# Performance work log

Measured on AMD Instinct MI355X. Metric: run time of the kernel, lower is better.

The kernel has to match this reference:

```python
import jax, jax.numpy as jnp
import numpy as np

B, S, D = 2, 4096, 768
H, DH = 12, 64
W = 256          # one-sided window (attention_window=512 // 2)
G = 8            # number of global tokens (first G positions)
NEG = -1e9


def setup_inputs() -> dict:
    key = jax.random.key(0)
    ks = jax.random.split(key, 8)
    hidden_states = jax.random.normal(ks[0], (B, S, D), dtype=jnp.float32)
    attention_mask = jnp.ones((B, S), dtype=jnp.float32)
    sc = 0.02
    Wq = jax.random.normal(ks[1], (D, D), dtype=jnp.float32) * sc
    Wk = jax.random.normal(ks[2], (D, D), dtype=jnp.float32) * sc
    Wv = jax.random.normal(ks[3], (D, D), dtype=jnp.float32) * sc
    Wqg = jax.random.normal(ks[4], (D, D), dtype=jnp.float32) * sc
    Wkg = jax.random.normal(ks[5], (D, D), dtype=jnp.float32) * sc
    Wvg = jax.random.normal(ks[6], (D, D), dtype=jnp.float32) * sc
    return {"hidden_states": hidden_states, "attention_mask": attention_mask,
            "Wq": Wq, "Wk": Wk, "Wv": Wv, "Wqg": Wqg, "Wkg": Wkg, "Wvg": Wvg}


def _heads(x):  # [B,S,D] -> [B,H,S,DH]
    return x.reshape(B, S, H, DH).transpose(0, 2, 1, 3)


def longformer_attn(hidden_states, attention_mask, Wq, Wk, Wv, Wqg, Wkg, Wvg):
    scale = 1.0 / jnp.sqrt(jnp.float32(DH))
    q = _heads(hidden_states @ Wq) * scale   # [B,H,S,DH]
    k = _heads(hidden_states @ Wk)
    v = _heads(hidden_states @ Wv)

    n = S // W                                # number of query chunks
    kp = jnp.pad(k, ((0, 0), (0, 0), (W, W), (0, 0)))
    vp = jnp.pad(v, ((0, 0), (0, 0), (W, W), (0, 0)))
    # window indices into padded seq: chunk i covers keys [i*W - W, i*W + 2W)
    idx = jnp.arange(n)[:, None] * W + jnp.arange(3 * W)[None, :]   # [n,3W]
    k_win = kp[:, :, idx]                     # [B,H,n,3W,DH]
    v_win = vp[:, :, idx]
    qc = q.reshape(B, H, n, W, DH)

    scores = jnp.einsum('bhnqd,bhnkd->bhnqk', qc, k_win)  # [B,H,n,W,3W]

    # masks: band (|key-query|<=W), valid key position, not a global key,
    # and key attention_mask
    rel = jnp.arange(3 * W)[None, :] - jnp.arange(W)[:, None]   # [W,3W] = k - q
    band = (rel >= 0) & (rel <= 2 * W)
    key_pos = idx - W                                           # [n,3W] real positions
    valid = (key_pos >= 0) & (key_pos < S) & (key_pos >= G)
    struct_mask = band[None, :, :] & valid[:, None, :]          # [n,W,3W]
    amp = jnp.pad(attention_mask, ((0, 0), (W, W)))
    am_win = amp[:, idx] > 0.5                                  # [B,n,3W]
    full_mask = struct_mask[None] & am_win[:, :, None, :]       # [B,n,W,3W]
    scores = jnp.where(full_mask[:, None], scores, NEG)

    # every query also attends to the G global keys (regular key projection)
    gk = k[:, :, :G]                                            # [B,H,G,DH]
    gscore = jnp.einsum('bhsd,bhgd->bhsg', q, gk).reshape(B, H, n, W, G)
    all_scores = jnp.concatenate([gscore, scores], axis=-1)     # [B,H,n,W,G+3W]
    probs = jax.nn.softmax(all_scores, axis=-1)

    gv = v[:, :, :G]
    out = (jnp.einsum('bhnqk,bhnkd->bhnqd', probs[..., G:], v_win)
           + jnp.einsum('bhnqg,bhgd->bhnqd', probs[..., :G], gv))
    out = out.reshape(B, H, S, DH)

    # global queries attend to ALL tokens with the *_global projections
    qg = _heads(hidden_states @ Wqg)[:, :, :G] * scale          # [B,H,G,DH]
    kg = _heads(hidden_states @ Wkg)
    vg = _heads(hidden_states @ Wvg)
    gs = jnp.einsum('bhgd,bhsd->bhgs', qg, kg)                  # [B,H,G,S]
    gs = jnp.where(attention_mask[:, None, None, :] > 0.5, gs, NEG)
    gp = jax.nn.softmax(gs, axis=-1)
    gout = jnp.einsum('bhgs,bhsd->bhgd', gp, vg)
    out = out.at[:, :, :G].set(gout)

    return out.transpose(0, 2, 1, 3).reshape(B, S, D)


def reference(hidden_states, attention_mask, Wq, Wk, Wv, Wqg, Wkg, Wvg):
    return longformer_attn(hidden_states, attention_mask, Wq, Wk, Wv, Wqg, Wkg, Wvg)
```

## Files before the change

kernel.cpp:

```cpp
#include <hip/hip_runtime.h>

#define B_ 2
#define S_ 4096
#define D_ 768
#define H_ 12
#define DH_ 64
#define W_ 256
#define G_ 8
#define NEG_ (-1e9f)
#define NC_ 64
#define CK_ 64
#define WQB 128
#define NT_ 11

typedef __attribute__((ext_vector_type(4))) float f32x4;
typedef __attribute__((ext_vector_type(16))) float f32x16;
typedef __attribute__((ext_vector_type(8))) short s16x8;
typedef __attribute__((ext_vector_type(4))) short s16x4;
typedef unsigned short ushort_t;

__device__ __forceinline__ unsigned short f2bf(float f) {
    union { float f; unsigned u; } v; v.f = f;
    unsigned r = v.u + 0x7FFFu + ((v.u >> 16) & 1u);
    return (unsigned short)(r >> 16);
}
__device__ __forceinline__ float bf2f(unsigned short b) {
    union { unsigned u; float f; } v; v.u = ((unsigned)b) << 16;
    return v.f;
}
__device__ __forceinline__ unsigned cvtpk_bf16(float lo, float hi) {
    unsigned r;
    asm("v_cvt_pk_bf16_f32 %0, %1, %2" : "=v"(r) : "v"(lo), "v"(hi));
    return r;
}
__device__ __forceinline__ void gload16(const ushort_t* g, ushort_t* l) {
    __builtin_amdgcn_global_load_lds(
        (const __attribute__((address_space(1))) unsigned*)g,
        (__attribute__((address_space(3))) unsigned*)l, 16, 0, 0);
}

__global__ __launch_bounds__(256) void convert_hs(const float* __restrict__ x,
                                                  ushort_t* __restrict__ y, int n8) {
    int i = blockIdx.x * 256 + threadIdx.x;
    if (i >= n8) return;
    float4 a = *(const float4*)&x[(size_t)i * 8];
    float4 c = *(const float4*)&x[(size_t)i * 8 + 4];
    s16x8 o;
    o[0] = (short)f2bf(a.x); o[1] = (short)f2bf(a.y);
    o[2] = (short)f2bf(a.z); o[3] = (short)f2bf(a.w);
    o[4] = (short)f2bf(c.x); o[5] = (short)f2bf(c.y);
    o[6] = (short)f2bf(c.z); o[7] = (short)f2bf(c.w);
    *(s16x8*)&y[(size_t)i * 8] = o;
}

__global__ __launch_bounds__(256) void convert_wt(const float* __restrict__ W0,
                                                  const float* __restrict__ W1,
                                                  const float* __restrict__ W2,
                                                  const float* __restrict__ W3,
                                                  const float* __restrict__ W4,
                                                  ushort_t* __restrict__ wt) {
    __shared__ float tile[32][33];
    const int w = blockIdx.z;
    const float* Wsrc = (w == 0) ? W0 : (w == 1) ? W1 : (w == 2) ? W2 : (w == 3) ? W3 : W4;
    const float scl = (w == 0) ? 0.125f : 1.0f;
    const int k0 = blockIdx.x * 32;
    const int n0 = blockIdx.y * 32;
    const int t = threadIdx.x;
    const int r = t >> 3, c4 = (t & 7) * 4;
    float4 src = *(const float4*)&Wsrc[(size_t)(k0 + r) * D_ + n0 + c4];
    tile[r][c4 + 0] = src.x; tile[r][c4 + 1] = src.y;
    tile[r][c4 + 2] = src.z; tile[r][c4 + 3] = src.w;
    __syncthreads();
    s16x4 o;
    o[0] = (short)f2bf(tile[c4 + 0][r] * scl);
    o[1] = (short)f2bf(tile[c4 + 1][r] * scl);
    o[2] = (short)f2bf(tile[c4 + 2][r] * scl);
    o[3] = (short)f2bf(tile[c4 + 3][r] * scl);
    *(s16x4*)&wt[((size_t)(w * D_ + n0 + r)) * D_ + k0 + c4] = o;
}

__global__ __launch_bounds__(256, 2) void proj_mfma(const ushort_t* __restrict__ A,
                                                    const ushort_t* __restrict__ Bt,
                                                    ushort_t* __restrict__ oq,
                                                    ushort_t* __restrict__ ok,
                                                    ushort_t* __restrict__ ov,
                                                    ushort_t* __restrict__ okg,
                                                    ushort_t* __restrict__ ovg) {
    __shared__ char smem[34048];
    ushort_t* Al = (ushort_t*)smem;
    ushort_t* Bl = Al + 128 * 64;

    const int t = threadIdx.x;
    const int m0 = blockIdx.x * 128;
    const int n0 = blockIdx.y * 128;
    const int lane = t & 63;
    const int w = t >> 6;
    const int wm = (w >> 1) * 64, wn = (w & 1) * 64;
    const int ln = lane & 15, hi = lane >> 4;

    const int srow_in_call = lane >> 3;
    const int scol = ((lane & 7) ^ srow_in_call) * 8;

    f32x4 acc[4][4];
#pragma unroll
    for (int mi = 0; mi < 4; ++mi)
#pragma unroll
        for (int ni = 0; ni < 4; ++ni) acc[mi][ni] = (f32x4){0.f, 0.f, 0.f, 0.f};

    for (int k0 = 0; k0 < D_; k0 += 64) {
        __syncthreads();
#pragma unroll
        for (int j = 0; j < 4; ++j) {
            const int rbase = (w * 4 + j) * 8;
            const int row = rbase + srow_in_call;
            gload16(&A[(size_t)(m0 + row) * D_ + k0 + scol], &Al[rbase * 64]);
            gload16(&Bt[(size_t)(n0 + row) * D_ + k0 + scol], &Bl[rbase * 64]);
        }
        __syncthreads();

#pragma unroll
        for (int ks = 0; ks < 2; ++ks) {
            s16x8 af[4], bf[4];
#pragma unroll
            for (int i = 0; i < 4; ++i) {
                const int ar = wm + i * 16 + ln;
                const int br = wn + i * 16 + ln;
                const int slot = (4 * ks + hi) ^ (ln & 7);
                af[i] = *(const s16x8*)&Al[ar * 64 + slot * 8];
                bf[i] = *(const s16x8*)&Bl[br * 64 + slot * 8];
            }
#pragma unroll
            for (int mi = 0; mi < 4; ++mi)
#pragma unroll
                for (int ni = 0; ni < 4; ++ni)
                    acc[mi][ni] = __builtin_amdgcn_mfma_f32_16x16x32_bf16(af[mi], bf[ni], acc[mi][ni], 0, 0, 0);
        }
    }

    float* scr = (float*)smem;
    const int rl = t >> 2, cs = (t & 3) * 32;
    const int ng = n0 + cs;
    const int w_idx = ng / D_;
    const int cb = ng - w_idx * D_;
    const int hh = cb >> 6, dd = cb & 63;
    ushort_t* dst = (w_idx == 0) ? oq : (w_idx == 1) ? ok : (w_idx == 2) ? ov
                    : (w_idx == 3) ? okg : ovg;

#pragma unroll
    for (int r = 0; r < 2; ++r) {
        __syncthreads();
        if ((w >> 1) == r) {
#pragma unroll
            for (int mi = 0; mi < 4; ++mi)
#pragma unroll
                for (int ni = 0; ni < 4; ++ni)
#pragma unroll
                    for (int rr = 0; rr < 4; ++rr)
                        scr[(mi * 16 + hi * 4 + rr) * 132 + wn + ni * 16 + ln] = acc[mi][ni][rr];
        }
        __syncthreads();
        const int m = m0 + r * 64 + rl;
        const int bb = m >> 12, s = m & 4095;
        ushort_t* drow = dst + ((size_t)(bb * H_ + hh) * S_ + s) * DH_ + dd;
        const float* srcp = scr + rl * 132 + cs;
#pragma unroll
        for (int seg = 0; seg < 4; ++seg) {
            float4 lo = *(const float4*)&srcp[seg * 8];
            float4 hi4 = *(const float4*)&srcp[seg * 8 + 4];
            s16x8 o;
            o[0] = (short)f2bf(lo.x); o[1] = (short)f2bf(lo.y);
            o[2] = (short)f2bf(lo.z); o[3] = (short)f2bf(lo.w);
            o[4] = (short)f2bf(hi4.x); o[5] = (short)f2bf(hi4.y);
            o[6] = (short)f2bf(hi4.z); o[7] = (short)f2bf(hi4.w);
            *(s16x8*)&drow[seg * 8] = o;
        }
    }
}

__global__ __launch_bounds__(256) void qg_gemm(const float* __restrict__ X,
                                               const float* __restrict__ Wm,
                                               float* __restrict__ qg) {
    const int rp = blockIdx.x;
    const int c0 = blockIdx.y * 128;
    const int t = threadIdx.x;
    const int r = t >> 7, cl = t & 127;
    __shared__ float xr[2][D_];
    for (int i = t; i < 2 * D_; i += 256) {
        const int rr = i / D_, kk = i - rr * D_;
        const int row = rp * 2 + rr;
        const int b = row >> 3, g = row & 7;
        xr[rr][kk] = X[((size_t)b * S_ + g) * D_ + kk];
    }
    __syncthreads();
    float a0 = 0.f, a1 = 0.f, a2 = 0.f, a3 = 0.f;
    const float* wp = &Wm[c0 + cl];
    for (int kk = 0; kk < D_; kk += 4) {
        a0 += xr[r][kk + 0] * wp[(size_t)(kk + 0) * D_];
        a1 += xr[r][kk + 1] * wp[(size_t)(kk + 1) * D_];
        a2 += xr[r][kk + 2] * wp[(size_t)(kk + 2) * D_];
        a3 += xr[r][kk + 3] * wp[(size_t)(kk + 3) * D_];
    }
    const int row = rp * 2 + r;
    qg[(size_t)row * D_ + c0 + cl] = (a0 + a1 + a2 + a3) * 0.125f;
}

__global__ __launch_bounds__(256, 2) void win_mfma(const ushort_t* __restrict__ q,
                                                   const ushort_t* __restrict__ k,
                                                   const ushort_t* __restrict__ v,
                                                   const float* __restrict__ am,
                                                   float* __restrict__ out) {
    __shared__ char smem[34816];
    ushort_t* Kl = (ushort_t*)smem;
    ushort_t* Vt = Kl + 64 * 72;
    unsigned* Mv = (unsigned*)(Vt + 64 * 66);
    float* Ow = (float*)smem;

    const int n = blockIdx.x, h = blockIdx.y, b = blockIdx.z;
    const int t = threadIdx.x;
    const int lane = t & 63, w = t >> 6;
    const int l31 = lane & 31, h5 = lane >> 5;
    const int q0w = n * WQB + w * 32;
    const int q_abs = q0w + l31;
    const size_t bh = (size_t)(b * H_ + h) * S_;

    s16x8 qf[4];
#pragma unroll
    for (int ks = 0; ks < 4; ++ks)
        qf[ks] = *(const s16x8*)&q[(bh + q_abs) * DH_ + ks * 16 + 8 * h5];

    f32x16 oacc[2];
#pragma unroll
    for (int dt = 0; dt < 2; ++dt)
#pragma unroll
        for (int i = 0; i < 16; ++i) oacc[dt][i] = 0.f;
    float m_run = -1e30f, l_run = 0.f;

    const int srow = t >> 2, soff = (t & 3) * 16;

    for (int tt = 0; tt < NT_; ++tt) {
        const bool isg = (tt == 0);
        const int pbase = n * WQB - W_ + (tt - 1) * 64;
        __syncthreads();
        {
            const int p = isg ? srow : pbase + srow;
            const int pr = p < 0 ? 0 : (p >= S_ ? S_ - 1 : p);
            const ushort_t* krow = &k[(bh + pr) * DH_ + soff];
            s16x8 k0v = *(const s16x8*)krow;
            s16x8 k1v = *(const s16x8*)(krow + 8);
            *(s16x8*)&Kl[srow * 72 + soff] = k0v;
            *(s16x8*)&Kl[srow * 72 + soff + 8] = k1v;
            const ushort_t* vrow = &v[(bh + pr) * DH_ + soff];
            s16x8 v0v = *(const s16x8*)vrow;
            s16x8 v1v = *(const s16x8*)(vrow + 8);
#pragma unroll
            for (int i = 0; i < 8; ++i) {
                Vt[(soff + i) * 66 + srow] = (ushort_t)v0v[i];
                Vt[(soff + 8 + i) * 66 + srow] = (ushort_t)v1v[i];
            }
        }
        if (w == 0) {
            const int p2 = isg ? lane : pbase + lane;
            const bool ok = isg ? (lane < G_)
                                : (p2 >= G_ && p2 < S_ && am[(size_t)b * S_ + p2] > 0.5f);
            unsigned long long bal = __ballot(ok);
            if (lane == 0) { Mv[0] = (unsigned)bal; Mv[1] = (unsigned)(bal >> 32); }
        }
        __syncthreads();

        if (!isg && (pbase > q0w + 31 + W_ || pbase + 63 < q0w - W_)) continue;

        f32x16 sc[2];
#pragma unroll
        for (int st = 0; st < 2; ++st)
#pragma unroll
            for (int i = 0; i < 16; ++i) sc[st][i] = 0.f;
#pragma unroll
        for (int st = 0; st < 2; ++st)
#pragma unroll
            for (int ks = 0; ks < 4; ++ks) {
                s16x8 kf = *(const s16x8*)&Kl[(st * 32 + l31) * 72 + ks * 16 + 8 * h5];
                sc[st] = __builtin_amdgcn_mfma_f32_32x32x16_bf16(kf, qf[ks], sc[st], 0, 0, 0);
            }

        const unsigned mv0 = Mv[0], mv1 = Mv[1];
        const bool fullt = !isg && ((mv0 & mv1) == 0xFFFFFFFFu) &&
                           (pbase >= q0w + 31 - W_) && (pbase + 63 <= q0w + W_);
        float tmax = -1e30f;
        if (fullt) {
#pragma unroll
            for (int st = 0; st < 2; ++st)
#pragma unroll
                for (int reg = 0; reg < 16; ++reg) tmax = fmaxf(tmax, sc[st][reg]);
        } else {
#pragma unroll
            for (int st = 0; st < 2; ++st)
#pragma unroll
                for (int reg = 0; reg < 16; ++reg) {
                    const int cst = (reg & 3) + 8 * (reg >> 2);
                    bool valid;
                    if (isg) {
                        valid = (st == 0) && (cst < 8);
                    } else {
                        const int crow = cst + 4 * h5;
                        const int key_abs = pbase + st * 32 + crow;
                        const unsigned mvx = (st == 0) ? mv0 : mv1;
                        valid = ((mvx >> crow) & 1u) &&
                                (key_abs >= q_abs - W_) && (key_abs <= q_abs + W_);
                    }
                    const float s = valid ? sc[st][reg] : -1e30f;
                    sc[st][reg] = s;
                    tmax = fmaxf(tmax, s);
                }
        }
        tmax = fmaxf(tmax, __shfl_xor(tmax, 32));

        if (__any(tmax > m_run + 8.f)) {
            const float mnew = fmaxf(m_run, tmax);
            const float f = __expf(m_run - mnew);
            l_run *= f;
#pragma unroll
            for (int dt = 0; dt < 2; ++dt)
#pragma unroll
                for (int i = 0; i < 16; ++i) oacc[dt][i] *= f;
            m_run = mnew;
        }
        float psum = 0.f;
#pragma unroll
        for (int st = 0; st < 2; ++st)
#pragma unroll
            for (int reg = 0; reg < 16; ++reg) {
                const float p = __expf(sc[st][reg] - m_run);
                sc[st][reg] = p;
                psum += p;
            }
        psum += __shfl_xor(psum, 32);
        l_run += psum;

#pragma unroll
        for (int ks = 0; ks < 4; ++ks) {
            const int st = ks >> 1, k8 = (ks & 1) * 8;
            const unsigned Au = cvtpk_bf16(sc[st][k8 + 0], sc[st][k8 + 1]);
            const unsigned Bu = cvtpk_bf16(sc[st][k8 + 2], sc[st][k8 + 3]);
            const unsigned Cu = cvtpk_bf16(sc[st][k8 + 4], sc[st][k8 + 5]);
            const unsigned Du = cvtpk_bf16(sc[st][k8 + 6], sc[st][k8 + 7]);
            const unsigned send0 = h5 ? Au : Cu;
            const unsigned send1 = h5 ? Bu : Du;
            const unsigned recv0 = __shfl_xor((int)send0, 32);
            const unsigned recv1 = __shfl_xor((int)send1, 32);
            union { unsigned u[4]; s16x8 v8; } pu;
            pu.u[0] = h5 ? recv0 : Au;
            pu.u[1] = h5 ? recv1 : Bu;
            pu.u[2] = h5 ? Cu : recv0;
            pu.u[3] = h5 ? Du : recv1;
#pragma unroll
            for (int dt = 0; dt < 2; ++dt) {
                const int vbase = (dt * 32 + l31) * 66 + ks * 16 + 8 * h5;
                union { unsigned u[4]; s16x8 v8; } vf;
                vf.u[0] = *(const unsigned*)&Vt[vbase + 0];
                vf.u[1] = *(const unsigned*)&Vt[vbase + 2];
                vf.u[2] = *(const unsigned*)&Vt[vbase + 4];
                vf.u[3] = *(const unsigned*)&Vt[vbase + 6];
                oacc[dt] = __builtin_amdgcn_mfma_f32_32x32x16_bf16(vf.v8, pu.v8, oacc[dt], 0, 0, 0);
            }
        }
    }

    __syncthreads();
    const float inv = 1.0f / l_run;
    float* OwW = Ow + w * 32 * 68;
#pragma unroll
    for (int dt = 0; dt < 2; ++dt)
#pragma unroll
        for (int reg = 0; reg < 16; ++reg) {
            const int d = dt * 32 + (reg & 3) + 8 * (reg >> 2) + 4 * h5;
            OwW[l31 * 68 + d] = oacc[dt][reg] * inv;
        }
    asm volatile("s_waitcnt lgkmcnt(0)" ::: "memory");
    const int qq = lane >> 1, half = lane & 1;
    const float* src = &OwW[qq * 68 + half * 32];
    float* dstp = &out[((size_t)b * S_ + q0w + qq) * D_ + h * DH_ + half * 32];
#pragma unroll
    for (int j = 0; j < 8; ++j)
        *(float4*)&dstp[j * 4] = *(const float4*)&src[j * 4];
}

__global__ __launch_bounds__(256) void glob_partial(const float* __restrict__ qg,
                                                    const ushort_t* __restrict__ kg,
                                                    const ushort_t* __restrict__ vg,
                                                    const float* __restrict__ am,
                                                    float* __restrict__ pout,
                                                    float* __restrict__ pm,
                                                    float* __restrict__ pl) {
    const int c = blockIdx.x, h = blockIdx.y, b = blockIdx.z;
    const int t = threadIdx.x;
    const int bh = b * H_ + h;
    const size_t base = (size_t)bh * S_ * DH_;
    const int jg0 = c * CK_;

    __shared__ float qs[G_][DH_];
    __shared__ float kt[CK_][69];
    __shared__ float vt[CK_][68];
    __shared__ float ps[G_][CK_];

    for (int i = t; i < G_ * DH_; i += 256)
        qs[i >> 6][i & 63] = qg[(size_t)(b * G_ + (i >> 6)) * D_ + h * DH_ + (i & 63)];
    {
        const int row = t >> 2, off = (t & 3) * 16;
        const ushort_t* kr = &kg[base + (size_t)(jg0 + row) * DH_ + off];
        const ushort_t* vr = &vg[base + (size_t)(jg0 + row) * DH_ + off];
        s16x8 ka = *(const s16x8*)kr;
        s16x8 kb2 = *(const s16x8*)(kr + 8);
        s16x8 va = *(const s16x8*)vr;
        s16x8 vb = *(const s16x8*)(vr + 8);
#pragma unroll
        for (int i = 0; i < 8; ++i) {
            kt[row][off + i] = bf2f((ushort_t)ka[i]);
            kt[row][off + 8 + i] = bf2f((ushort_t)kb2[i]);
            vt[row][off + i] = bf2f((ushort_t)va[i]);
            vt[row][off + 8 + i] = bf2f((ushort_t)vb[i]);
        }
    }
    __syncthreads();

    const int g = t >> 5, jl = t & 31;
    float sc0 = 0.f, sc1 = 0.f;
#pragma unroll 8
    for (int d = 0; d < DH_; ++d) {
        const float qv = qs[g][d];
        sc0 += qv * kt[jl][d];
        sc1 += qv * kt[jl + 32][d];
    }
    if (!(am[(size_t)b * S_ + jg0 + jl] > 0.5f)) sc0 = NEG_;
    if (!(am[(size_t)b * S_ + jg0 + jl + 32] > 0.5f)) sc1 = NEG_;

    float mm = fmaxf(sc0, sc1);
    mm = fmaxf(mm, __shfl_xor(mm, 1));
    mm = fmaxf(mm, __shfl_xor(mm, 2));
    mm = fmaxf(mm, __shfl_xor(mm, 4));
    mm = fmaxf(mm, __shfl_xor(mm, 8));
    mm = fmaxf(mm, __shfl_xor(mm, 16));
    const float p0 = __expf(sc0 - mm);
    const float p1 = __expf(sc1 - mm);
    float ls = p0 + p1;
    ls += __shfl_xor(ls, 1);
    ls += __shfl_xor(ls, 2);
    ls += __shfl_xor(ls, 4);
    ls += __shfl_xor(ls, 8);
    ls += __shfl_xor(ls, 16);
    ps[g][jl] = p0;
    ps[g][jl + 32] = p1;
    if (jl == 0) {
        pm[((size_t)bh * NC_ + c) * G_ + g] = mm;
        pl[((size_t)bh * NC_ + c) * G_ + g] = ls;
    }
    __syncthreads();

#pragma unroll
    for (int pass = 0; pass < 2; ++pass) {
        const int gg = (t >> 6) + pass * 4;
        const int d = t & 63;
        float acc = 0.f;
#pragma unroll 8
        for (int j = 0; j < CK_; ++j) acc += ps[gg][j] * vt[j][d];
        pout[(((size_t)bh * NC_ + c) * G_ + gg) * DH_ + d] = acc;
    }
}

__global__ __launch_bounds__(256) void glob_reduce(const float* __restrict__ pout,
                                                   const float* __restrict__ pm,
                                                   const float* __restrict__ pl,
                                                   float* __restrict__ out) {
    const int bh = blockIdx.x;
    const int b = bh / H_, h = bh - b * H_;
    const int t = threadIdx.x;

    __shared__ float wc[G_][NC_];
    __shared__ float wsum[G_];

    const int g = t >> 5, cl = t & 31;
    const float m0 = pm[((size_t)bh * NC_ + cl) * G_ + g];
    const float m1 = pm[((size_t)bh * NC_ + cl + 32) * G_ + g];
    float M = fmaxf(m0, m1);
    M = fmaxf(M, __shfl_xor(M, 1));
    M = fmaxf(M, __shfl_xor(M, 2));
    M = fmaxf(M, __shfl_xor(M, 4));
    M = fmaxf(M, __shfl_xor(M, 8));
    M = fmaxf(M, __shfl_xor(M, 16));
    const float w0 = __expf(m0 - M);
    const float w1 = __expf(m1 - M);
    float S = w0 * pl[((size_t)bh * NC_ + cl) * G_ + g] +
              w1 * pl[((size_t)bh * NC_ + cl + 32) * G_ + g];
    S += __shfl_xor(S, 1);
    S += __shfl_xor(S, 2);
    S += __shfl_xor(S, 4);
    S += __shfl_xor(S, 8);
    S += __shfl_xor(S, 16);
    wc[g][cl] = w0;
    wc[g][cl + 32] = w1;
    if (cl == 0) wsum[g] = S;
    __syncthreads();

#pragma unroll
    for (int pass = 0; pass < 2; ++pass) {
        const int gg = (t >> 6) + pass * 4;
        const int d = t & 63;
        float acc = 0.f;
        for (int c2 = 0; c2 < NC_; ++c2)
            acc += wc[gg][c2] * pout[(((size_t)bh * NC_ + c2) * G_ + gg) * DH_ + d];
        out[((size_t)b * S_ + gg) * D_ + h * DH_ + d] = acc / wsum[gg];
    }
}

extern "C" void kernel_launch(void* const* d_in, const int* in_sizes, int n_in,
                              void* d_out, int out_size, void* d_ws, size_t ws_size,
                              hipStream_t stream) {
    (void)in_sizes; (void)n_in; (void)out_size; (void)ws_size;

    const float* hs    = (const float*)d_in[0];
    const float* amask = (const float*)d_in[1];
    const float* Wq    = (const float*)d_in[2];
    const float* Wk    = (const float*)d_in[3];
    const float* Wv    = (const float*)d_in[4];
    const float* Wqg   = (const float*)d_in[5];
    const float* Wkg   = (const float*)d_in[6];
    const float* Wvg   = (const float*)d_in[7];
    float* out = (float*)d_out;

    char* p = (char*)d_ws;
    ushort_t* hs_bf = (ushort_t*)p; p += (size_t)B_ * S_ * D_ * 2;
    ushort_t* wt    = (ushort_t*)p; p += (size_t)5 * D_ * D_ * 2;
    const size_t per = (size_t)B_ * H_ * S_ * DH_;
    ushort_t* qb  = (ushort_t*)p; p += per * 2;
    ushort_t* kb  = (ushort_t*)p; p += per * 2;
    ushort_t* vb  = (ushort_t*)p; p += per * 2;
    ushort_t* kgb = (ushort_t*)p; p += per * 2;
    ushort_t* vgb = (ushort_t*)p; p += per * 2;
    float* qg   = (float*)p; p += (size_t)B_ * G_ * D_ * 4;
    float* pout = (float*)p; p += (size_t)B_ * H_ * NC_ * G_ * DH_ * 4;
    float* pm   = (float*)p; p += (size_t)B_ * H_ * NC_ * G_ * 4;
    float* pl   = (float*)p;

    convert_hs<<<(B_ * S_ * D_ / 8 + 255) / 256, 256, 0, stream>>>(hs, hs_bf, B_ * S_ * D_ / 8);
    convert_wt<<<dim3(D_ / 32, D_ / 32, 5), 256, 0, stream>>>(Wq, Wk, Wv, Wkg, Wvg, wt);
    proj_mfma<<<dim3(B_ * S_ / 128, 5 * D_ / 128), 256, 0, stream>>>(hs_bf, wt, qb, kb, vb, kgb, vgb);
    qg_gemm<<<dim3(B_ * G_ / 2, D_ / 128), 256, 0, stream>>>(hs, Wqg, qg);
    win_mfma<<<dim3(S_ / WQB, H_, B_), 256, 0, stream>>>(qb, kb, vb, amask, out);
    glob_partial<<<dim3(NC_, H_, B_), 256, 0, stream>>>(qg, kgb, vgb, amask, pout, pm, pl);
    glob_reduce<<<B_ * H_, 256, 0, stream>>>(pout, pm, pl, out);
}
```

Before: 154.3 us.

## Rewrite projection GEMM as 256x256 double-buffered 8-wave pipelined kernel

The projection GEMM moves from 128x128 tiles with 4 waves and a single LDS buffer to 256x256 tiles with 8 waves, double-buffered LDS, and global loads for the next k-tile interleaved between four MFMA phases. Explicit barriers, waitcnt and setprio are used to overlap the memory traffic with the matrix-core work. Block IDs are remapped so consecutive blocks are spread across the grid for better L2 locality. The larger tile raises data reuse, but a 128KB LDS footprint and a 32-tile accumulator raise register and LDS pressure, and the launch-bounds occupancy of 2 blocks per CU may not be reachable.

```diff
diff --git a/kernel.cpp b/kernel.cpp
--- a/kernel.cpp
+++ b/kernel.cpp
@@ -12,6 +12,7 @@
 #define CK_ 64
 #define WQB 128
 #define NT_ 11
+#define KT_ 12
 
 typedef __attribute__((ext_vector_type(4))) float f32x4;
 typedef __attribute__((ext_vector_type(16))) float f32x16;
@@ -79,94 +80,176 @@
     *(s16x4*)&wt[((size_t)(w * D_ + n0 + r)) * D_ + k0 + c4] = o;
 }
 
-__global__ __launch_bounds__(256, 2) void proj_mfma(const ushort_t* __restrict__ A,
+#define LGKM0 do { asm volatile("s_waitcnt lgkmcnt(0)" ::: "memory"); \
+                   __builtin_amdgcn_sched_barrier(0); } while (0)
+
+#define STAGE2(kt, hh) do {                                                   \
+    const int isB_ = (hh) >> 1, hf_ = (hh) & 1;                               \
+    const ushort_t* gb_ = isB_ ? Bt : A;                                      \
+    const int rb_ = isB_ ? n0 : m0;                                           \
+    _Pragma("unroll")                                                         \
+    for (int c_ = 0; c_ < 2; ++c_) {                                          \
+        const int rw_ = hf_ * 128 + c_ * 64 + w * 8;                          \
+        gload16(gb_ + (size_t)(rb_ + rw_ + srow8) * D_ + (kt) * 64 + scol,    \
+                &lds[((kt) & 1) * 32768 + isB_ * 16384 + rw_ * 64]);          \
+    } } while (0)
+
+#define LDSRD(baseEl, row, slot) \
+    (*(const s16x8*)&lds[(baseEl) + (row) * 64 + (((slot) ^ ((row) & 7)) * 8)])
+
+__global__ __launch_bounds__(512, 2) void proj_mfma(const ushort_t* __restrict__ A,
                                                     const ushort_t* __restrict__ Bt,
                                                     ushort_t* __restrict__ oq,
                                                     ushort_t* __restrict__ ok,
                                                     ushort_t* __restrict__ ov,
                                                     ushort_t* __restrict__ okg,
                                                     ushort_t* __restrict__ ovg) {
-    __shared__ char smem[34048];
-    ushort_t* Al = (ushort_t*)smem;
-    ushort_t* Bl = Al + 128 * 64;
+    __shared__ ushort_t lds[65536];
 
     const int t = threadIdx.x;
-    const int m0 = blockIdx.x * 128;
-    const int n0 = blockIdx.y * 128;
-    const int lane = t & 63;
-    const int w = t >> 6;
-    const int wm = (w >> 1) * 64, wn = (w & 1) * 64;
+    const int lane = t & 63, w = t >> 6;
     const int ln = lane & 15, hi = lane >> 4;
-
-    const int srow_in_call = lane >> 3;
-    const int scol = ((lane & 7) ^ srow_in_call) * 8;
-
-    f32x4 acc[4][4];
-#pragma unroll
-    for (int mi = 0; mi < 4; ++mi)
-#pragma unroll
-        for (int ni = 0; ni < 4; ++ni) acc[mi][ni] = (f32x4){0.f, 0.f, 0.f, 0.f};
-
-    for (int k0 = 0; k0 < D_; k0 += 64) {
+    const int wm = (w >> 2) * 128, wn = (w & 3) * 64;
+
+    int bid = blockIdx.x;
+    bid = (bid & 7) * 60 + (bid >> 3);
+    const int bx = bid / 15, by = bid % 15;
+    const int m0 = bx * 256, n0 = by * 256;
+
+    const int srow8 = lane >> 3;
+    const int scol = ((lane & 7) ^ srow8) * 8;
+
+    f32x4 acc[8][4];
+#pragma unroll
+    for (int i = 0; i < 8; ++i)
+#pragma unroll
+        for (int j = 0; j < 4; ++j) acc[i][j] = (f32x4){0.f, 0.f, 0.f, 0.f};
+
+    s16x8 a[4][2], bb_[4][2];
+
+    STAGE2(0, 0); STAGE2(0, 1); STAGE2(0, 2); STAGE2(0, 3);
+    STAGE2(1, 0); STAGE2(1, 1);
+    asm volatile("s_waitcnt vmcnt(4)" ::: "memory");
+    __builtin_amdgcn_s_barrier();
+
+    for (int kt = 0; kt < KT_; ++kt) {
+        const int Ab = (kt & 1) * 32768;
+        const int Bb = Ab + 16384;
+
+#pragma unroll
+        for (int i = 0; i < 4; ++i)
+#pragma unroll
+            for (int ks = 0; ks < 2; ++ks)
+                a[i][ks] = LDSRD(Ab, wm + i * 16 + ln, ks * 4 + hi);
+#pragma unroll
+        for (int i = 0; i < 2; ++i)
+#pragma unroll
+            for (int ks = 0; ks < 2; ++ks)
+                bb_[i][ks] = LDSRD(Bb, wn + i * 16 + ln, ks * 4 + hi);
+        if (kt < KT_ - 1) STAGE2(kt + 1, 2);
+        __builtin_amdgcn_s_barrier();
+        LGKM0;
+        __builtin_amdgcn_s_setprio(1);
+#pragma unroll
+        for (int mi = 0; mi < 4; ++mi)
+#pragma unroll
+            for (int ni = 0; ni < 2; ++ni) {
+                acc[mi][ni] = __builtin_amdgcn_mfma_f32_16x16x32_bf16(a[mi][0], bb_[ni][0], acc[mi][ni], 0, 0, 0);
+                acc[mi][ni] = __builtin_amdgcn_mfma_f32_16x16x32_bf16(a[mi][1], bb_[ni][1], acc[mi][ni], 0, 0, 0);
+            }
+        __builtin_amdgcn_s_setprio(0);
+        __builtin_amdgcn_s_barrier();
+
+#pragma unroll
+        for (int i = 2; i < 4; ++i)
+#pragma unroll
+            for (int ks = 0; ks < 2; ++ks)
+                bb_[i][ks] = LDSRD(Bb, wn + i * 16 + ln, ks * 4 + hi);
+        if (kt < KT_ - 1) STAGE2(kt + 1, 3);
+        __builtin_amdgcn_s_barrier();
+        LGKM0;
+        __builtin_amdgcn_s_setprio(1);
+#pragma unroll
+        for (int mi = 0; mi < 4; ++mi)
+#pragma unroll
+            for (int ni = 2; ni < 4; ++ni) {
+                acc[mi][ni] = __builtin_amdgcn_mfma_f32_16x16x32_bf16(a[mi][0], bb_[ni][0], acc[mi][ni], 0, 0, 0);
+                acc[mi][ni] = __builtin_amdgcn_mfma_f32_16x16x32_bf16(a[mi][1], bb_[ni][1], acc[mi][ni], 0, 0, 0);
+            }
+        __builtin_amdgcn_s_setprio(0);
+        __builtin_amdgcn_s_barrier();
+
+#pragma unroll
+        for (int i = 0; i < 4; ++i)
+#pragma unroll
+            for (int ks = 0; ks < 2; ++ks)
+                a[i][ks] = LDSRD(Ab, wm + 64 + i * 16 + ln, ks * 4 + hi);
+        __builtin_amdgcn_s_barrier();
+        LGKM0;
+        __builtin_amdgcn_s_setprio(1);
+#pragma unroll
+        for (int mi = 0; mi < 4; ++mi)
+#pragma unroll
+            for (int ni = 0; ni < 2; ++ni) {
+                acc[4 + mi][ni] = __builtin_amdgcn_mfma_f32_16x16x32_bf16(a[mi][0], bb_[ni][0], acc[4 + mi][ni], 0, 0, 0);
+                acc[4 + mi][ni] = __builtin_amdgcn_mfma_f32_16x16x32_bf16(a[mi][1], bb_[ni][1], acc[4 + mi][ni], 0, 0, 0);
+            }
+        __builtin_amdgcn_s_setprio(0);
+        __builtin_amdgcn_s_barrier();
+
+        if (kt < KT_ - 2) { STAGE2(kt + 2, 0); STAGE2(kt + 2, 1); }
+        __builtin_amdgcn_s_barrier();
+        __builtin_amdgcn_s_setprio(1);
+#pragma unroll
+        for (int mi = 0; mi < 4; ++mi)
+#pragma unroll
+            for (int ni = 2; ni < 4; ++ni) {
+                acc[4 + mi][ni] = __builtin_amdgcn_mfma_f32_16x16x32_bf16(a[mi][0], bb_[ni][0], acc[4 + mi][ni], 0, 0, 0);
+                acc[4 + mi][ni] = __builtin_amdgcn_mfma_f32_16x16x32_bf16(a[mi][1], bb_[ni][1], acc[4 + mi][ni], 0, 0, 0);
+            }
+        __builtin_amdgcn_s_setprio(0);
+        __builtin_amdgcn_s_barrier();
+
+        if (kt < KT_ - 1) {
+            if (kt == KT_ - 2) asm volatile("s_waitcnt vmcnt(0)" ::: "memory");
+            else               asm volatile("s_waitcnt vmcnt(4)" ::: "memory");
+            __builtin_amdgcn_s_barrier();
+        }
+    }
+
+    float* scr = (float*)lds;
+    const int lr_w = t >> 3;
+    const int cseg = (t & 7) * 32;
+    const int wi = by / 3;
+    const int cb0 = (by % 3) * 256;
+    ushort_t* dst = (wi == 0) ? oq : (wi == 1) ? ok : (wi == 2) ? ov
+                    : (wi == 3) ? okg : ovg;
+    const int cc = cb0 + cseg;
+    const int hh2 = cc >> 6, dd = cc & 63;
+
+#pragma unroll
+    for (int r = 0; r < 4; ++r) {
         __syncthreads();
-#pragma unroll
-        for (int j = 0; j < 4; ++j) {
-            const int rbase = (w * 4 + j) * 8;
-            const int row = rbase + srow_in_call;
-            gload16(&A[(size_t)(m0 + row) * D_ + k0 + scol], &Al[rbase * 64]);
-            gload16(&Bt[(size_t)(n0 + row) * D_ + k0 + scol], &Bl[rbase * 64]);
+        if ((w >> 2) == (r >> 1)) {
+#pragma unroll
+            for (int i = 0; i < 4; ++i) {
+                const int mi = (r & 1) * 4 + i;
+#pragma unroll
+                for (int ni = 0; ni < 4; ++ni)
+#pragma unroll
+                    for (int rr = 0; rr < 4; ++rr)
+                        scr[(i * 16 + hi * 4 + rr) * 268 + wn + ni * 16 + ln] = acc[mi][ni][rr];
+            }
         }
         __syncthreads();
-
-#pragma unroll
-        for (int ks = 0; ks < 2; ++ks) {
-            s16x8 af[4], bf[4];
-#pragma unroll
-            for (int i = 0; i < 4; ++i) {
-                const int ar = wm + i * 16 + ln;
-                const int br = wn + i * 16 + ln;
-                const int slot = (4 * ks + hi) ^ (ln & 7);
-                af[i] = *(const s16x8*)&Al[ar * 64 + slot * 8];
-                bf[i] = *(const s16x8*)&Bl[br * 64 + slot * 8];
-            }
-#pragma unroll
-            for (int mi = 0; mi < 4; ++mi)
-#pragma unroll
-                for (int ni = 0; ni < 4; ++ni)
-                    acc[mi][ni] = __builtin_amdgcn_mfma_f32_16x16x32_bf16(af[mi], bf[ni], acc[mi][ni], 0, 0, 0);
-        }
-    }
-
-    float* scr = (float*)smem;
-    const int rl = t >> 2, cs = (t & 3) * 32;
-    const int ng = n0 + cs;
-    const int w_idx = ng / D_;
-    const int cb = ng - w_idx * D_;
-    const int hh = cb >> 6, dd = cb & 63;
-    ushort_t* dst = (w_idx == 0) ? oq : (w_idx == 1) ? ok : (w_idx == 2) ? ov
-                    : (w_idx == 3) ? okg : ovg;
-
-#pragma unroll
-    for (int r = 0; r < 2; ++r) {
-        __syncthreads();
-        if ((w >> 1) == r) {
-#pragma unroll
-            for (int mi = 0; mi < 4; ++mi)
-#pragma unroll
-                for (int ni = 0; ni < 4; ++ni)
-#pragma unroll
-                    for (int rr = 0; rr < 4; ++rr)
-                        scr[(mi * 16 + hi * 4 + rr) * 132 + wn + ni * 16 + ln] = acc[mi][ni][rr];
-        }
-        __syncthreads();
-        const int m = m0 + r * 64 + rl;
-        const int bb = m >> 12, s = m & 4095;
-        ushort_t* drow = dst + ((size_t)(bb * H_ + hh) * S_ + s) * DH_ + dd;
-        const float* srcp = scr + rl * 132 + cs;
+        const int m = m0 + r * 64 + lr_w;
+        const int bbk = m >> 12, s = m & 4095;
+        ushort_t* drow = dst + ((size_t)(bbk * H_ + hh2) * S_ + s) * DH_ + dd;
+        const float* sp = scr + lr_w * 268 + cseg;
 #pragma unroll
         for (int seg = 0; seg < 4; ++seg) {
-            float4 lo = *(const float4*)&srcp[seg * 8];
-            float4 hi4 = *(const float4*)&srcp[seg * 8 + 4];
+            float4 lo = *(const float4*)&sp[seg * 8];
+            float4 hi4 = *(const float4*)&sp[seg * 8 + 4];
             s16x8 o;
             o[0] = (short)f2bf(lo.x); o[1] = (short)f2bf(lo.y);
             o[2] = (short)f2bf(lo.z); o[3] = (short)f2bf(lo.w);
@@ -542,7 +625,7 @@
 
     convert_hs<<<(B_ * S_ * D_ / 8 + 255) / 256, 256, 0, stream>>>(hs, hs_bf, B_ * S_ * D_ / 8);
     convert_wt<<<dim3(D_ / 32, D_ / 32, 5), 256, 0, stream>>>(Wq, Wk, Wv, Wkg, Wvg, wt);
-    proj_mfma<<<dim3(B_ * S_ / 128, 5 * D_ / 128), 256, 0, stream>>>(hs_bf, wt, qb, kb, vb, kgb, vgb);
+    proj_mfma<<<480, 512, 0, stream>>>(hs_bf, wt, qb, kb, vb, kgb, vgb);
     qg_gemm<<<dim3(B_ * G_ / 2, D_ / 128), 256, 0, stream>>>(hs, Wqg, qg);
     win_mfma<<<dim3(S_ / WQB, H_, B_), 256, 0, stream>>>(qb, kb, vb, amask, out);
     glob_partial<<<dim3(NC_, H_, B_), 256, 0, stream>>>(qg, kgb, vgb, amask, pout, pm, pl);
```

Result: slower. 159.9 us (+3.6%).

## Prefetch next K/V tile into registers, peel global-token tile, use exp2 softmax

Applied to the files above, without the earlier changes.

The global-key tile is peeled out of the attention loop and handled with a specialized 4-register softmax path. The loop now register-prefetches the next window tile's K, V and mask while the current tile is being computed, so global-load latency overlaps with the MFMA work. The 1/sqrt(d) query scale is folded with log2(e) so the kernel can use exp2f instead of __expf, and the lazy rescale threshold is widened to match the base-2 scale. This costs more live registers, which may lower occupancy.

```diff
diff --git a/kernel.cpp b/kernel.cpp
--- a/kernel.cpp
+++ b/kernel.cpp
@@ -62,7 +62,7 @@
     __shared__ float tile[32][33];
     const int w = blockIdx.z;
     const float* Wsrc = (w == 0) ? W0 : (w == 1) ? W1 : (w == 2) ? W2 : (w == 3) ? W3 : W4;
-    const float scl = (w == 0) ? 0.125f : 1.0f;
+    const float scl = (w == 0) ? 0.125f * 1.44269504f : 1.0f;
     const int k0 = blockIdx.x * 32;
     const int n0 = blockIdx.y * 32;
     const int t = threadIdx.x;
@@ -233,41 +233,118 @@
     for (int dt = 0; dt < 2; ++dt)
 #pragma unroll
         for (int i = 0; i < 16; ++i) oacc[dt][i] = 0.f;
-    float m_run = -1e30f, l_run = 0.f;
+    float m_run, l_run;
 
     const int srow = t >> 2, soff = (t & 3) * 16;
-
-    for (int tt = 0; tt < NT_; ++tt) {
-        const bool isg = (tt == 0);
+    s16x8 kreg0, kreg1, vreg0, vreg1;
+    float amv = 0.f;
+
+    {
+        const ushort_t* krow = &k[(bh + srow) * DH_ + soff];
+        kreg0 = *(const s16x8*)krow;
+        kreg1 = *(const s16x8*)(krow + 8);
+        const ushort_t* vrow = &v[(bh + srow) * DH_ + soff];
+        vreg0 = *(const s16x8*)vrow;
+        vreg1 = *(const s16x8*)(vrow + 8);
+        *(s16x8*)&Kl[srow * 72 + soff] = kreg0;
+        *(s16x8*)&Kl[srow * 72 + soff + 8] = kreg1;
+#pragma unroll
+        for (int i = 0; i < 8; ++i) {
+            Vt[(soff + i) * 66 + srow] = (ushort_t)vreg0[i];
+            Vt[(soff + 8 + i) * 66 + srow] = (ushort_t)vreg1[i];
+        }
+    }
+    __syncthreads();
+
+    {
+        const int p = n * WQB - W_ + srow;
+        const int pr = p < 0 ? 0 : p;
+        const ushort_t* krow = &k[(bh + pr) * DH_ + soff];
+        kreg0 = *(const s16x8*)krow;
+        kreg1 = *(const s16x8*)(krow + 8);
+        const ushort_t* vrow = &v[(bh + pr) * DH_ + soff];
+        vreg0 = *(const s16x8*)vrow;
+        vreg1 = *(const s16x8*)(vrow + 8);
+        if (w == 0) {
+            const int p2 = n * WQB - W_ + lane;
+            amv = (p2 >= 0 && p2 < S_) ? am[(size_t)b * S_ + p2] : 0.f;
+        }
+    }
+
+    {
+        f32x16 s0;
+#pragma unroll
+        for (int i = 0; i < 16; ++i) s0[i] = 0.f;
+#pragma unroll
+        for (int ks = 0; ks < 4; ++ks) {
+            s16x8 kf = *(const s16x8*)&Kl[l31 * 72 + ks * 16 + 8 * h5];
+            s0 = __builtin_amdgcn_mfma_f32_32x32x16_bf16(kf, qf[ks], s0, 0, 0, 0);
+        }
+        float tmax = fmaxf(fmaxf(s0[0], s0[1]), fmaxf(s0[2], s0[3]));
+        tmax = fmaxf(tmax, __shfl_xor(tmax, 32));
+        m_run = tmax;
+        float p0 = exp2f(s0[0] - m_run), p1 = exp2f(s0[1] - m_run);
+        float p2 = exp2f(s0[2] - m_run), p3 = exp2f(s0[3] - m_run);
+        float psum = p0 + p1 + p2 + p3;
+        psum += __shfl_xor(psum, 32);
+        l_run = psum;
+        const unsigned Au = cvtpk_bf16(p0, p1);
+        const unsigned Bu = cvtpk_bf16(p2, p3);
+        const unsigned send0 = h5 ? Au : 0u;
+        const unsigned send1 = h5 ? Bu : 0u;
+        const unsigned recv0 = __shfl_xor((int)send0, 32);
+        const unsigned recv1 = __shfl_xor((int)send1, 32);
+        union { unsigned u[4]; s16x8 v8; } pu;
+        pu.u[0] = h5 ? recv0 : Au;
+        pu.u[1] = h5 ? recv1 : Bu;
+        pu.u[2] = h5 ? 0u : recv0;
+        pu.u[3] = h5 ? 0u : recv1;
+#pragma unroll
+        for (int dt = 0; dt < 2; ++dt) {
+            const int vbase = (dt * 32 + l31) * 66 + 8 * h5;
+            union { unsigned u[4]; s16x8 v8; } vf;
+            vf.u[0] = *(const unsigned*)&Vt[vbase + 0];
+            vf.u[1] = *(const unsigned*)&Vt[vbase + 2];
+            vf.u[2] = *(const unsigned*)&Vt[vbase + 4];
+            vf.u[3] = *(const unsigned*)&Vt[vbase + 6];
+            oacc[dt] = __builtin_amdgcn_mfma_f32_32x32x16_bf16(vf.v8, pu.v8, oacc[dt], 0, 0, 0);
+        }
+    }
+
+    for (int tt = 1; tt < NT_; ++tt) {
         const int pbase = n * WQB - W_ + (tt - 1) * 64;
         __syncthreads();
-        {
-            const int p = isg ? srow : pbase + srow;
+        *(s16x8*)&Kl[srow * 72 + soff] = kreg0;
+        *(s16x8*)&Kl[srow * 72 + soff + 8] = kreg1;
+#pragma unroll
+        for (int i = 0; i < 8; ++i) {
+            Vt[(soff + i) * 66 + srow] = (ushort_t)vreg0[i];
+            Vt[(soff + 8 + i) * 66 + srow] = (ushort_t)vreg1[i];
+        }
+        if (w == 0) {
+            const int p2 = pbase + lane;
+            const bool ok = (p2 >= G_ && p2 < S_ && amv > 0.5f);
+            unsigned long long bal = __ballot(ok);
+            if (lane == 0) { Mv[0] = (unsigned)bal; Mv[1] = (unsigned)(bal >> 32); }
+        }
+        __syncthreads();
+
+        if (tt < NT_ - 1) {
+            const int p = pbase + 64 + srow;
             const int pr = p < 0 ? 0 : (p >= S_ ? S_ - 1 : p);
             const ushort_t* krow = &k[(bh + pr) * DH_ + soff];
-            s16x8 k0v = *(const s16x8*)krow;
-            s16x8 k1v = *(const s16x8*)(krow + 8);
-            *(s16x8*)&Kl[srow * 72 + soff] = k0v;
-            *(s16x8*)&Kl[srow * 72 + soff + 8] = k1v;
+            kreg0 = *(const s16x8*)krow;
+            kreg1 = *(const s16x8*)(krow + 8);
             const ushort_t* vrow = &v[(bh + pr) * DH_ + soff];
-            s16x8 v0v = *(const s16x8*)vrow;
-            s16x8 v1v = *(const s16x8*)(vrow + 8);
-#pragma unroll
-            for (int i = 0; i < 8; ++i) {
-                Vt[(soff + i) * 66 + srow] = (ushort_t)v0v[i];
-                Vt[(soff + 8 + i) * 66 + srow] = (ushort_t)v1v[i];
+            vreg0 = *(const s16x8*)vrow;
+            vreg1 = *(const s16x8*)(vrow + 8);
+            if (w == 0) {
+                const int p2 = pbase + 64 + lane;
+                amv = (p2 >= 0 && p2 < S_) ? am[(size_t)b * S_ + p2] : 0.f;
             }
         }
-        if (w == 0) {
-            const int p2 = isg ? lane : pbase + lane;
-            const bool ok = isg ? (lane < G_)
-                                : (p2 >= G_ && p2 < S_ && am[(size_t)b * S_ + p2] > 0.5f);
-            unsigned long long bal = __ballot(ok);
-            if (lane == 0) { Mv[0] = (unsigned)bal; Mv[1] = (unsigned)(bal >> 32); }
-        }
-        __syncthreads();
-
-        if (!isg && (pbase > q0w + 31 + W_ || pbase + 63 < q0w - W_)) continue;
+
+        if (pbase > q0w + 31 + W_ || pbase + 63 < q0w - W_) continue;
 
         f32x16 sc[2];
 #pragma unroll
@@ -283,7 +360,7 @@
             }
 
         const unsigned mv0 = Mv[0], mv1 = Mv[1];
-        const bool fullt = !isg && ((mv0 & mv1) == 0xFFFFFFFFu) &&
+        const bool fullt = ((mv0 & mv1) == 0xFFFFFFFFu) &&
                            (pbase >= q0w + 31 - W_) && (pbase + 63 <= q0w + W_);
         float tmax = -1e30f;
         if (fullt) {
@@ -297,16 +374,11 @@
 #pragma unroll
                 for (int reg = 0; reg < 16; ++reg) {
                     const int cst = (reg & 3) + 8 * (reg >> 2);
-                    bool valid;
-                    if (isg) {
-                        valid = (st == 0) && (cst < 8);
-                    } else {
-                        const int crow = cst + 4 * h5;
-                        const int key_abs = pbase + st * 32 + crow;
-                        const unsigned mvx = (st == 0) ? mv0 : mv1;
-                        valid = ((mvx >> crow) & 1u) &&
-                                (key_abs >= q_abs - W_) && (key_abs <= q_abs + W_);
-                    }
+                    const int crow = cst + 4 * h5;
+                    const int key_abs = pbase + st * 32 + crow;
+                    const unsigned mvx = (st == 0) ? mv0 : mv1;
+                    const bool valid = ((mvx >> crow) & 1u) &&
+                                       (key_abs >= q_abs - W_) && (key_abs <= q_abs + W_);
                     const float s = valid ? sc[st][reg] : -1e30f;
                     sc[st][reg] = s;
                     tmax = fmaxf(tmax, s);
@@ -314,9 +386,9 @@
         }
         tmax = fmaxf(tmax, __shfl_xor(tmax, 32));
 
-        if (__any(tmax > m_run + 8.f)) {
+        if (__any(tmax > m_run + 11.5f)) {
             const float mnew = fmaxf(m_run, tmax);
-            const float f = __expf(m_run - mnew);
+            const float f = exp2f(m_run - mnew);
             l_run *= f;
 #pragma unroll
             for (int dt = 0; dt < 2; ++dt)
@@ -329,7 +401,7 @@
         for (int st = 0; st < 2; ++st)
 #pragma unroll
             for (int reg = 0; reg < 16; ++reg) {
-                const float p = __expf(sc[st][reg] - m_run);
+                const float p = exp2f(sc[st][reg] - m_run);
                 sc[st][reg] = p;
                 psum += p;
             }
```

Result: slower. 157.8 us (+2.3%).
